# Kernel tuning notes

Measured on AMD Instinct MI355X. Metric: run time of the kernel, lower is better.

The kernel has to match this reference:

```python
import jax, jax.numpy as jnp
import numpy as np

BETA = 0.25

def setup_inputs() -> dict:
    key = jax.random.key(0)
    k1, k2 = jax.random.split(key)
    z = jax.random.normal(k1, (32, 64, 64, 64), dtype=jnp.float32)  # (B, D, H, W)
    # EmbeddingEMA init: uniform(-1/K, 1/K)
    K, D = 1024, 64
    weight = jax.random.uniform(k2, (K, D), dtype=jnp.float32, minval=-1.0 / K, maxval=1.0 / K)
    return {"z": z, "weight": weight}


def reference(z, weight):
    b, d, h, w = z.shape
    K = weight.shape[0]
    # permute (B,D,H,W) -> (B,H,W,D) and flatten to (N, D)
    z_flat = jnp.transpose(z, (0, 2, 3, 1)).reshape(-1, d)
    # squared euclidean distance: ||z||^2 + ||c||^2 - 2 z c^T  -> (N, K)
    distance = (
        jnp.sum(z_flat * z_flat, axis=1, keepdims=True)
        + jnp.sum(weight * weight, axis=1)
        - 2.0 * jnp.matmul(z_flat, weight.T)
    )
    vq_indices = jnp.argmin(distance, axis=1)  # (N,)
    z_quantized = weight[vq_indices]  # gather (N, D)
    # one-hot scatter stats (training-time EMA inputs)
    vq_current_count = jax.ops.segment_sum(
        jnp.ones((z_flat.shape[0],), dtype=z_flat.dtype), vq_indices, num_segments=K)
    vq_current_sum = jax.ops.segment_sum(z_flat, vq_indices, num_segments=K)  # (K, D)
    commitment_loss = jnp.mean((z_flat - jax.lax.stop_gradient(z_quantized)) ** 2)
    loss = BETA * commitment_loss
    # straight-through estimator
    q = z_flat + jax.lax.stop_gradient(z_quantized - z_flat)
    q = jnp.transpose(q.reshape(b, h, w, d), (0, 3, 1, 2))  # back to (B, D, H, W)
    return q, loss, commitment_loss, vq_current_count, vq_current_sum
```

## Files before the change

kernel.cpp:

```cpp
#include <hip/hip_runtime.h>


#define HWsz   4096
#define Dd     64
#define Kk     1024
#define NB     32
#define NTOT   131072
#define QSIZE  (NTOT * Dd)
#define BETA_C 0.25f

typedef float  f32x4  __attribute__((ext_vector_type(4)));
typedef short  bf16x8 __attribute__((ext_vector_type(8)));

__device__ __forceinline__ unsigned short f2bf(float f) {
    unsigned u = __float_as_uint(f);
    u += 0x7FFF + ((u >> 16) & 1);
    return (unsigned short)(u >> 16);
}
__device__ __forceinline__ float bf2f(unsigned short b) {
    return __uint_as_float(((unsigned)b) << 16);
}

__global__ __launch_bounds__(256) void vq_prep(const float* __restrict__ w,
                                               float* __restrict__ c2,
                                               unsigned short* __restrict__ whi,
                                               unsigned short* __restrict__ wlo) {
    int t = blockIdx.x * 256 + threadIdx.x;
    int k = t >> 6, d = t & 63;
    float v = w[t];
    unsigned short hb = f2bf(v);
    unsigned short lb = f2bf(v - bf2f(hb));
    int ctile = k >> 4, col = k & 15;
    int s = d >> 5, kg = (d >> 3) & 3, j = d & 7;
    int idx = (((ctile * 2 + s) * 64) + kg * 16 + col) * 8 + j;
    whi[idx] = hb; wlo[idx] = lb;

    if (t < Kk) {
        const float4* c4 = reinterpret_cast<const float4*>(w + t * Dd);
        float s0 = 0.f, s1 = 0.f, s2 = 0.f, s3 = 0.f;
#pragma unroll
        for (int q = 0; q < 16; ++q) {
            float4 cq = c4[q];
            s0 = fmaf(cq.x, cq.x, s0); s1 = fmaf(cq.y, cq.y, s1);
            s2 = fmaf(cq.z, cq.z, s2); s3 = fmaf(cq.w, cq.w, s3);
        }
        c2[t] = (s0 + s1) + (s2 + s3);
    }
}

__global__ __launch_bounds__(256) void vq_dist(const float* __restrict__ z,
                                               const float* __restrict__ w,
                                               const float* __restrict__ c2,
                                               const unsigned short* __restrict__ whi,
                                               const unsigned short* __restrict__ wlo,
                                               float* __restrict__ out,
                                               float* __restrict__ accum,
                                               int* __restrict__ idx_ws) {
    const int lane = threadIdx.x & 63;
    const int wid  = threadIdx.x >> 6;
    const int b    = blockIdx.x >> 4;
    const int t0   = (blockIdx.x & 15) * 16 + wid * 4;
    const int col  = lane & 15;
    const int kg   = lane >> 4;

    bf16x8 zhi[4][2], zlo[4][2];
#pragma unroll
    for (int m = 0; m < 4; ++m) {
        const int hw0 = (t0 + m) << 4;
        const float* zbase = z + (size_t)b * (Dd * HWsz) + hw0 + col;
#pragma unroll
        for (int s = 0; s < 2; ++s) {
            bf16x8 h, l;
#pragma unroll
            for (int j = 0; j < 8; ++j) {
                float zz = zbase[(size_t)(32 * s + kg * 8 + j) * HWsz];
                unsigned short hb = f2bf(zz);
                unsigned short lb = f2bf(zz - bf2f(hb));
                h[j] = (short)hb; l[j] = (short)lb;
            }
            zhi[m][s] = h; zlo[m][s] = l;
        }
    }

    float best[4][4];
    int   bk[4][4];
#pragma unroll
    for (int m = 0; m < 4; ++m)
#pragma unroll
        for (int r = 0; r < 4; ++r) { best[m][r] = 3.4e38f; bk[m][r] = 0; }

    const bf16x8* ph = reinterpret_cast<const bf16x8*>(whi);
    const bf16x8* pl = reinterpret_cast<const bf16x8*>(wlo);

    for (int ct = 0; ct < 64; ++ct) {
        bf16x8 wh0 = ph[(ct * 2 + 0) * 64 + lane];
        bf16x8 wh1 = ph[(ct * 2 + 1) * 64 + lane];
        bf16x8 wl0 = pl[(ct * 2 + 0) * 64 + lane];
        bf16x8 wl1 = pl[(ct * 2 + 1) * 64 + lane];

        float cv = c2[ct * 16 + col];
        int   kc = ct * 16 + col;

#pragma unroll
        for (int m = 0; m < 4; ++m) {
            f32x4 za = {0.f, 0.f, 0.f, 0.f};
            f32x4 zb = {0.f, 0.f, 0.f, 0.f};
            za = __builtin_amdgcn_mfma_f32_16x16x32_bf16(zhi[m][0], wh0, za, 0, 0, 0);
            za = __builtin_amdgcn_mfma_f32_16x16x32_bf16(zhi[m][1], wh1, za, 0, 0, 0);
            za = __builtin_amdgcn_mfma_f32_16x16x32_bf16(zhi[m][0], wl0, za, 0, 0, 0);
            za = __builtin_amdgcn_mfma_f32_16x16x32_bf16(zhi[m][1], wl1, za, 0, 0, 0);
            zb = __builtin_amdgcn_mfma_f32_16x16x32_bf16(zlo[m][0], wh0, zb, 0, 0, 0);
            zb = __builtin_amdgcn_mfma_f32_16x16x32_bf16(zlo[m][1], wh1, zb, 0, 0, 0);
#pragma unroll
            for (int r = 0; r < 4; ++r) {
                float s = fmaf(-2.f, za[r] + zb[r], cv);
                if (s < best[m][r]) { best[m][r] = s; bk[m][r] = kc; }
            }
        }
    }

#pragma unroll
    for (int off = 1; off < 16; off <<= 1) {
#pragma unroll
        for (int m = 0; m < 4; ++m)
#pragma unroll
            for (int r = 0; r < 4; ++r) {
                float ob = __shfl_xor(best[m][r], off, 64);
                int   ok = __shfl_xor(bk[m][r],   off, 64);
                if (ob < best[m][r] || (ob == best[m][r] && ok < bk[m][r])) {
                    best[m][r] = ob; bk[m][r] = ok;
                }
            }
    }

    float commit = 0.f;
    const int srcl = (col >> 2) << 4;
    const int rsel = col & 3;
#pragma unroll
    for (int m = 0; m < 4; ++m) {
        int c0 = __shfl(bk[m][0], srcl, 64);
        int c1 = __shfl(bk[m][1], srcl, 64);
        int c2r = __shfl(bk[m][2], srcl, 64);
        int c3 = __shfl(bk[m][3], srcl, 64);
        int mybk = (rsel == 0) ? c0 : (rsel == 1) ? c1 : (rsel == 2) ? c2r : c3;

        const int hw0 = (t0 + m) << 4;
        if (lane < 16) idx_ws[(size_t)b * HWsz + hw0 + col] = mybk;

        float* qbase = out + (size_t)b * (Dd * HWsz) + hw0 + col;
#pragma unroll
        for (int s = 0; s < 2; ++s) {
            const float4* cw = reinterpret_cast<const float4*>(w + mybk * Dd + 32 * s + kg * 8);
            float4 p0 = cw[0], p1 = cw[1];
            float cb[8] = {p0.x, p0.y, p0.z, p0.w, p1.x, p1.y, p1.z, p1.w};
#pragma unroll
            for (int j = 0; j < 8; ++j) {
                int   d  = 32 * s + kg * 8 + j;
                float zz = bf2f((unsigned short)zhi[m][s][j]) +
                           bf2f((unsigned short)zlo[m][s][j]);
                float cc = cb[j];
                qbase[(size_t)d * HWsz] = zz + (cc - zz);
                float dd = zz - cc;
                commit = fmaf(dd, dd, commit);
            }
        }
    }

#pragma unroll
    for (int off = 32; off > 0; off >>= 1) commit += __shfl_down(commit, off, 64);

    __shared__ float red[4];
    if (lane == 0) red[wid] = commit;
    __syncthreads();
    if (threadIdx.x == 0)
        atomicAdd(accum, (red[0] + red[1]) + (red[2] + red[3]));
}

__global__ __launch_bounds__(256) void vq_stats(const float* __restrict__ z,
                                                const int* __restrict__ idx_ws,
                                                float* __restrict__ psum,
                                                float* __restrict__ pcnt) {
    const int b     = blockIdx.x >> 3;
    const int chunk = blockIdx.x & 7;
    const int dbase = chunk * 8;
    const bool docnt = (chunk == 0);

    __shared__ float acc[8][Kk];
    __shared__ float cnt[Kk];
    for (int i = threadIdx.x; i < 8 * Kk; i += 256)
        acc[i >> 10][i & 1023] = 0.f;
    for (int i = threadIdx.x; i < Kk; i += 256) cnt[i] = 0.f;
    __syncthreads();

    const int4* ip = reinterpret_cast<const int4*>(idx_ws + (size_t)b * HWsz);
#pragma unroll
    for (int it = 0; it < 4; ++it) {
        int c4 = it * 256 + threadIdx.x;
        int4 k4 = ip[c4];
#pragma unroll
        for (int d8 = 0; d8 < 8; ++d8) {
            const float4 v4 = reinterpret_cast<const float4*>(
                z + ((size_t)b * Dd + dbase + d8) * HWsz)[c4];
            atomicAdd(&acc[d8][k4.x], v4.x);
            atomicAdd(&acc[d8][k4.y], v4.y);
            atomicAdd(&acc[d8][k4.z], v4.z);
            atomicAdd(&acc[d8][k4.w], v4.w);
        }
        if (docnt) {
            atomicAdd(&cnt[k4.x], 1.f);
            atomicAdd(&cnt[k4.y], 1.f);
            atomicAdd(&cnt[k4.z], 1.f);
            atomicAdd(&cnt[k4.w], 1.f);
        }
    }
    __syncthreads();

    float* po = psum + (size_t)b * (Dd * Kk) + (size_t)dbase * Kk;
    for (int i = threadIdx.x; i < 8 * Kk; i += 256)
        po[i] = acc[i >> 10][i & 1023];
    if (docnt) {
        float* pc = pcnt + (size_t)b * Kk;
        for (int i = threadIdx.x; i < Kk; i += 256) pc[i] = cnt[i];
    }
}

__global__ __launch_bounds__(256) void vq_reduce(const float* __restrict__ psum,
                                                 const float* __restrict__ pcnt,
                                                 const float* __restrict__ accum,
                                                 float* __restrict__ out) {
    int t = blockIdx.x * 256 + threadIdx.x;
    int k = t & 1023, d = t >> 10;
    float s = 0.f;
#pragma unroll
    for (int b = 0; b < NB; ++b)
        s += psum[(size_t)b * (Dd * Kk) + (size_t)d * Kk + k];
    out[QSIZE + 2 + Kk + (size_t)k * Dd + d] = s;
    if (t < Kk) {
        float c = 0.f;
#pragma unroll
        for (int b = 0; b < NB; ++b) c += pcnt[((size_t)b << 10) + t];
        out[QSIZE + 2 + t] = c;
    }
    if (t == 0) {
        float c = accum[0] / (float)QSIZE;
        out[QSIZE]     = BETA_C * c;
        out[QSIZE + 1] = c;
    }
}

extern "C" void kernel_launch(void* const* d_in, const int* in_sizes, int n_in,
                              void* d_out, int out_size, void* d_ws, size_t ws_size,
                              hipStream_t stream) {
    const float* z = (const float*)d_in[0];
    const float* w = (const float*)d_in[1];
    float* out = (float*)d_out;

    float* accum = (float*)d_ws;
    float* c2    = (float*)d_ws + 64;
    unsigned short* whi = (unsigned short*)((float*)d_ws + 64 + Kk);
    unsigned short* wlo = whi + (Kk * Dd);
    int*   idx_ws = (int*)(wlo + (Kk * Dd));
    float* psum   = (float*)(idx_ws + NTOT);
    float* pcnt   = psum + (size_t)NB * Dd * Kk;

    hipMemsetAsync(accum, 0, 64 * sizeof(float), stream);

    vq_prep<<<(Kk * Dd) / 256, 256, 0, stream>>>(w, c2, whi, wlo);
    vq_dist<<<NTOT / 256, 256, 0, stream>>>(z, w, c2, whi, wlo, out, accum, idx_ws);
    vq_stats<<<NB * 8, 256, 0, stream>>>(z, idx_ws, psum, pcnt);
    vq_reduce<<<(Kk * Dd) / 256, 256, 0, stream>>>(psum, pcnt, accum, out);
}
```

Baseline: 243.0 us.

## Stage codebook in LDS with double buffering and restructure dist/stats kernels

The distance kernel now runs 128-thread blocks that double-buffer the split-bf16 codebook chunks into LDS via global_load_lds. It interleaves MFMAs across four independent accumulators for more instruction-level parallelism and drops the separate zlo accumulator. The global atomic plus memset for the commitment loss is replaced by per-block partials reduced in the final kernel. The stats kernel is split finer, two D channels per block, giving more blocks and less LDS per block. This trades extra barriers and smaller blocks for less global-load latency on the codebook and better occupancy.

```diff
diff --git a/kernel.cpp b/kernel.cpp
--- a/kernel.cpp
+++ b/kernel.cpp
@@ -8,6 +8,8 @@
 #define NTOT   131072
 #define QSIZE  (NTOT * Dd)
 #define BETA_C 0.25f
+#define DIST_BLOCKS 1024
+#define NCHUNK 16
 
 typedef float  f32x4  __attribute__((ext_vector_type(4)));
 typedef short  bf16x8 __attribute__((ext_vector_type(8)));
@@ -19,6 +21,16 @@
 }
 __device__ __forceinline__ float bf2f(unsigned short b) {
     return __uint_as_float(((unsigned)b) << 16);
+}
+
+__device__ __forceinline__ void stage16(const void* g, void* lds, int lane) {
+#if __has_builtin(__builtin_amdgcn_global_load_lds)
+    __builtin_amdgcn_global_load_lds(
+        (const __attribute__((address_space(1))) unsigned int*)g,
+        (__attribute__((address_space(3))) unsigned int*)lds, 16, 0, 0);
+#else
+    *(bf16x8*)((unsigned short*)lds + lane * 8) = *(const bf16x8*)g;
+#endif
 }
 
 __global__ __launch_bounds__(256) void vq_prep(const float* __restrict__ w,
@@ -48,26 +60,27 @@
     }
 }
 
-__global__ __launch_bounds__(256) void vq_dist(const float* __restrict__ z,
-                                               const float* __restrict__ w,
-                                               const float* __restrict__ c2,
-                                               const unsigned short* __restrict__ whi,
-                                               const unsigned short* __restrict__ wlo,
-                                               float* __restrict__ out,
-                                               float* __restrict__ accum,
-                                               int* __restrict__ idx_ws) {
+__global__ __launch_bounds__(128, 3) void vq_dist(const float* __restrict__ z,
+                                                  const float* __restrict__ w,
+                                                  const float* __restrict__ c2,
+                                                  const unsigned short* __restrict__ whi,
+                                                  const unsigned short* __restrict__ wlo,
+                                                  float* __restrict__ out,
+                                                  float* __restrict__ commit_ws,
+                                                  int* __restrict__ idx_ws) {
     const int lane = threadIdx.x & 63;
     const int wid  = threadIdx.x >> 6;
-    const int b    = blockIdx.x >> 4;
-    const int t0   = (blockIdx.x & 15) * 16 + wid * 4;
+    const int b    = blockIdx.x >> 5;
+    const int hwb  = (blockIdx.x & 31) * 128 + wid * 64;
     const int col  = lane & 15;
     const int kg   = lane >> 4;
 
+    __shared__ unsigned short lbuf[2][8192];
+
     bf16x8 zhi[4][2], zlo[4][2];
 #pragma unroll
     for (int m = 0; m < 4; ++m) {
-        const int hw0 = (t0 + m) << 4;
-        const float* zbase = z + (size_t)b * (Dd * HWsz) + hw0 + col;
+        const float* zbase = z + (size_t)b * (Dd * HWsz) + (hwb + m * 16) + col;
 #pragma unroll
         for (int s = 0; s < 2; ++s) {
             bf16x8 h, l;
@@ -82,6 +95,19 @@
         }
     }
 
+    const char* ghi = (const char*)whi;
+    const char* glo = (const char*)wlo;
+#define STAGE(c, bufi)                                                          \
+    {                                                                           \
+        unsigned short* dst = lbuf[bufi];                                       \
+        _Pragma("unroll")                                                       \
+        for (int rd = 0; rd < 4; ++rd) {                                        \
+            int rec = ((c) * 8 + rd * 2 + wid) * 1024 + lane * 16;              \
+            stage16(ghi + rec, dst + rd * 2048 + wid * 512, lane);              \
+            stage16(glo + rec, dst + rd * 2048 + (2 + wid) * 512, lane);        \
+        }                                                                       \
+    }
+
     float best[4][4];
     int   bk[4][4];
 #pragma unroll
@@ -89,34 +115,53 @@
 #pragma unroll
         for (int r = 0; r < 4; ++r) { best[m][r] = 3.4e38f; bk[m][r] = 0; }
 
-    const bf16x8* ph = reinterpret_cast<const bf16x8*>(whi);
-    const bf16x8* pl = reinterpret_cast<const bf16x8*>(wlo);
-
-    for (int ct = 0; ct < 64; ++ct) {
-        bf16x8 wh0 = ph[(ct * 2 + 0) * 64 + lane];
-        bf16x8 wh1 = ph[(ct * 2 + 1) * 64 + lane];
-        bf16x8 wl0 = pl[(ct * 2 + 0) * 64 + lane];
-        bf16x8 wl1 = pl[(ct * 2 + 1) * 64 + lane];
-
-        float cv = c2[ct * 16 + col];
-        int   kc = ct * 16 + col;
-
-#pragma unroll
-        for (int m = 0; m < 4; ++m) {
-            f32x4 za = {0.f, 0.f, 0.f, 0.f};
-            f32x4 zb = {0.f, 0.f, 0.f, 0.f};
-            za = __builtin_amdgcn_mfma_f32_16x16x32_bf16(zhi[m][0], wh0, za, 0, 0, 0);
-            za = __builtin_amdgcn_mfma_f32_16x16x32_bf16(zhi[m][1], wh1, za, 0, 0, 0);
-            za = __builtin_amdgcn_mfma_f32_16x16x32_bf16(zhi[m][0], wl0, za, 0, 0, 0);
-            za = __builtin_amdgcn_mfma_f32_16x16x32_bf16(zhi[m][1], wl1, za, 0, 0, 0);
-            zb = __builtin_amdgcn_mfma_f32_16x16x32_bf16(zlo[m][0], wh0, zb, 0, 0, 0);
-            zb = __builtin_amdgcn_mfma_f32_16x16x32_bf16(zlo[m][1], wh1, zb, 0, 0, 0);
-#pragma unroll
-            for (int r = 0; r < 4; ++r) {
-                float s = fmaf(-2.f, za[r] + zb[r], cv);
-                if (s < best[m][r]) { best[m][r] = s; bk[m][r] = kc; }
-            }
-        }
+    STAGE(0, 0);
+    __syncthreads();
+
+    for (int c = 0; c < NCHUNK; ++c) {
+        const unsigned short* cb = lbuf[c & 1];
+        if (c + 1 < NCHUNK) STAGE(c + 1, (c + 1) & 1);
+#pragma unroll
+        for (int t = 0; t < 4; ++t) {
+            const int ct = c * 4 + t;
+            bf16x8 wh0 = *(const bf16x8*)(cb + t * 2048 + 0 * 512 + lane * 8);
+            bf16x8 wh1 = *(const bf16x8*)(cb + t * 2048 + 1 * 512 + lane * 8);
+            bf16x8 wl0 = *(const bf16x8*)(cb + t * 2048 + 2 * 512 + lane * 8);
+            bf16x8 wl1 = *(const bf16x8*)(cb + t * 2048 + 3 * 512 + lane * 8);
+            const float cv = c2[ct * 16 + col];
+            const int   kc = ct * 16 + col;
+
+            f32x4 za[4];
+#pragma unroll
+            for (int m = 0; m < 4; ++m) za[m] = (f32x4){0.f, 0.f, 0.f, 0.f};
+#pragma unroll
+            for (int m = 0; m < 4; ++m)
+                za[m] = __builtin_amdgcn_mfma_f32_16x16x32_bf16(zhi[m][0], wh0, za[m], 0, 0, 0);
+#pragma unroll
+            for (int m = 0; m < 4; ++m)
+                za[m] = __builtin_amdgcn_mfma_f32_16x16x32_bf16(zhi[m][1], wh1, za[m], 0, 0, 0);
+#pragma unroll
+            for (int m = 0; m < 4; ++m)
+                za[m] = __builtin_amdgcn_mfma_f32_16x16x32_bf16(zhi[m][0], wl0, za[m], 0, 0, 0);
+#pragma unroll
+            for (int m = 0; m < 4; ++m)
+                za[m] = __builtin_amdgcn_mfma_f32_16x16x32_bf16(zhi[m][1], wl1, za[m], 0, 0, 0);
+#pragma unroll
+            for (int m = 0; m < 4; ++m)
+                za[m] = __builtin_amdgcn_mfma_f32_16x16x32_bf16(zlo[m][0], wh0, za[m], 0, 0, 0);
+#pragma unroll
+            for (int m = 0; m < 4; ++m)
+                za[m] = __builtin_amdgcn_mfma_f32_16x16x32_bf16(zlo[m][1], wh1, za[m], 0, 0, 0);
+
+#pragma unroll
+            for (int m = 0; m < 4; ++m)
+#pragma unroll
+                for (int r = 0; r < 4; ++r) {
+                    float s = fmaf(-2.f, za[m][r], cv);
+                    if (s < best[m][r]) { best[m][r] = s; bk[m][r] = kc; }
+                }
+        }
+        __syncthreads();
     }
 
 #pragma unroll
@@ -144,7 +189,7 @@
         int c3 = __shfl(bk[m][3], srcl, 64);
         int mybk = (rsel == 0) ? c0 : (rsel == 1) ? c1 : (rsel == 2) ? c2r : c3;
 
-        const int hw0 = (t0 + m) << 4;
+        const int hw0 = hwb + m * 16;
         if (lane < 16) idx_ws[(size_t)b * HWsz + hw0 + col] = mybk;
 
         float* qbase = out + (size_t)b * (Dd * HWsz) + hw0 + col;
@@ -152,13 +197,13 @@
         for (int s = 0; s < 2; ++s) {
             const float4* cw = reinterpret_cast<const float4*>(w + mybk * Dd + 32 * s + kg * 8);
             float4 p0 = cw[0], p1 = cw[1];
-            float cb[8] = {p0.x, p0.y, p0.z, p0.w, p1.x, p1.y, p1.z, p1.w};
+            float cbv[8] = {p0.x, p0.y, p0.z, p0.w, p1.x, p1.y, p1.z, p1.w};
 #pragma unroll
             for (int j = 0; j < 8; ++j) {
                 int   d  = 32 * s + kg * 8 + j;
                 float zz = bf2f((unsigned short)zhi[m][s][j]) +
                            bf2f((unsigned short)zlo[m][s][j]);
-                float cc = cb[j];
+                float cc = cbv[j];
                 qbase[(size_t)d * HWsz] = zz + (cc - zz);
                 float dd = zz - cc;
                 commit = fmaf(dd, dd, commit);
@@ -169,55 +214,47 @@
 #pragma unroll
     for (int off = 32; off > 0; off >>= 1) commit += __shfl_down(commit, off, 64);
 
-    __shared__ float red[4];
+    __shared__ float red[2];
     if (lane == 0) red[wid] = commit;
     __syncthreads();
-    if (threadIdx.x == 0)
-        atomicAdd(accum, (red[0] + red[1]) + (red[2] + red[3]));
+    if (threadIdx.x == 0) commit_ws[blockIdx.x] = red[0] + red[1];
 }
 
 __global__ __launch_bounds__(256) void vq_stats(const float* __restrict__ z,
                                                 const int* __restrict__ idx_ws,
                                                 float* __restrict__ psum,
                                                 float* __restrict__ pcnt) {
-    const int b     = blockIdx.x >> 3;
-    const int chunk = blockIdx.x & 7;
-    const int dbase = chunk * 8;
-    const bool docnt = (chunk == 0);
-
-    __shared__ float acc[8][Kk];
-    __shared__ float cnt[Kk];
-    for (int i = threadIdx.x; i < 8 * Kk; i += 256)
-        acc[i >> 10][i & 1023] = 0.f;
-    for (int i = threadIdx.x; i < Kk; i += 256) cnt[i] = 0.f;
+    const int b  = blockIdx.x >> 5;
+    const int dp = blockIdx.x & 31;
+    const int d0 = dp * 2;
+    const bool docnt = (dp == 0);
+
+    __shared__ float acc0[Kk], acc1[Kk], cnt[Kk];
+    for (int i = threadIdx.x; i < Kk; i += 256) { acc0[i] = 0.f; acc1[i] = 0.f; cnt[i] = 0.f; }
     __syncthreads();
 
-    const int4* ip = reinterpret_cast<const int4*>(idx_ws + (size_t)b * HWsz);
+    const int4*   ip  = reinterpret_cast<const int4*>(idx_ws + (size_t)b * HWsz);
+    const float4* zp0 = reinterpret_cast<const float4*>(z + ((size_t)b * Dd + d0) * HWsz);
+    const float4* zp1 = reinterpret_cast<const float4*>(z + ((size_t)b * Dd + d0 + 1) * HWsz);
 #pragma unroll
     for (int it = 0; it < 4; ++it) {
         int c4 = it * 256 + threadIdx.x;
-        int4 k4 = ip[c4];
-#pragma unroll
-        for (int d8 = 0; d8 < 8; ++d8) {
-            const float4 v4 = reinterpret_cast<const float4*>(
-                z + ((size_t)b * Dd + dbase + d8) * HWsz)[c4];
-            atomicAdd(&acc[d8][k4.x], v4.x);
-            atomicAdd(&acc[d8][k4.y], v4.y);
-            atomicAdd(&acc[d8][k4.z], v4.z);
-            atomicAdd(&acc[d8][k4.w], v4.w);
-        }
+        int4   k4 = ip[c4];
+        float4 v0 = zp0[c4];
+        float4 v1 = zp1[c4];
+        atomicAdd(&acc0[k4.x], v0.x); atomicAdd(&acc0[k4.y], v0.y);
+        atomicAdd(&acc0[k4.z], v0.z); atomicAdd(&acc0[k4.w], v0.w);
+        atomicAdd(&acc1[k4.x], v1.x); atomicAdd(&acc1[k4.y], v1.y);
+        atomicAdd(&acc1[k4.z], v1.z); atomicAdd(&acc1[k4.w], v1.w);
         if (docnt) {
-            atomicAdd(&cnt[k4.x], 1.f);
-            atomicAdd(&cnt[k4.y], 1.f);
-            atomicAdd(&cnt[k4.z], 1.f);
-            atomicAdd(&cnt[k4.w], 1.f);
+            atomicAdd(&cnt[k4.x], 1.f); atomicAdd(&cnt[k4.y], 1.f);
+            atomicAdd(&cnt[k4.z], 1.f); atomicAdd(&cnt[k4.w], 1.f);
         }
     }
     __syncthreads();
 
-    float* po = psum + (size_t)b * (Dd * Kk) + (size_t)dbase * Kk;
-    for (int i = threadIdx.x; i < 8 * Kk; i += 256)
-        po[i] = acc[i >> 10][i & 1023];
+    float* po = psum + ((size_t)b * Dd + d0) * Kk;
+    for (int i = threadIdx.x; i < Kk; i += 256) { po[i] = acc0[i]; po[Kk + i] = acc1[i]; }
     if (docnt) {
         float* pc = pcnt + (size_t)b * Kk;
         for (int i = threadIdx.x; i < Kk; i += 256) pc[i] = cnt[i];
@@ -226,14 +263,14 @@
 
 __global__ __launch_bounds__(256) void vq_reduce(const float* __restrict__ psum,
                                                  const float* __restrict__ pcnt,
-                                                 const float* __restrict__ accum,
+                                                 const float* __restrict__ commit_ws,
                                                  float* __restrict__ out) {
     int t = blockIdx.x * 256 + threadIdx.x;
     int k = t & 1023, d = t >> 10;
     float s = 0.f;
 #pragma unroll
     for (int b = 0; b < NB; ++b)
-        s += psum[(size_t)b * (Dd * Kk) + (size_t)d * Kk + k];
+        s += psum[((size_t)b * Dd + d) * Kk + k];
     out[QSIZE + 2 + Kk + (size_t)k * Dd + d] = s;
     if (t < Kk) {
         float c = 0.f;
@@ -241,10 +278,21 @@
         for (int b = 0; b < NB; ++b) c += pcnt[((size_t)b << 10) + t];
         out[QSIZE + 2 + t] = c;
     }
-    if (t == 0) {
-        float c = accum[0] / (float)QSIZE;
-        out[QSIZE]     = BETA_C * c;
-        out[QSIZE + 1] = c;
+
+    if (blockIdx.x == 0) {
+        float cs = 0.f;
+        for (int i = threadIdx.x; i < DIST_BLOCKS; i += 256) cs += commit_ws[i];
+#pragma unroll
+        for (int off = 32; off > 0; off >>= 1) cs += __shfl_down(cs, off, 64);
+        __shared__ float r2[4];
+        const int lane = threadIdx.x & 63, wid = threadIdx.x >> 6;
+        if (lane == 0) r2[wid] = cs;
+        __syncthreads();
+        if (threadIdx.x == 0) {
+            float c = ((r2[0] + r2[1]) + (r2[2] + r2[3])) / (float)QSIZE;
+            out[QSIZE]     = BETA_C * c;
+            out[QSIZE + 1] = c;
+        }
     }
 }
 
@@ -255,18 +303,16 @@
     const float* w = (const float*)d_in[1];
     float* out = (float*)d_out;
 
-    float* accum = (float*)d_ws;
-    float* c2    = (float*)d_ws + 64;
-    unsigned short* whi = (unsigned short*)((float*)d_ws + 64 + Kk);
+    float* commit_ws = (float*)d_ws;
+    float* c2        = (float*)d_ws + 1024;
+    unsigned short* whi = (unsigned short*)((float*)d_ws + 2048);
     unsigned short* wlo = whi + (Kk * Dd);
     int*   idx_ws = (int*)(wlo + (Kk * Dd));
-    float* psum   = (float*)(idx_ws + NTOT);
-    float* pcnt   = psum + (size_t)NB * Dd * Kk;
-
-    hipMemsetAsync(accum, 0, 64 * sizeof(float), stream);
+    float* pcnt   = (float*)(idx_ws + NTOT);
+    float* psum   = pcnt + (size_t)NB * Kk;
 
     vq_prep<<<(Kk * Dd) / 256, 256, 0, stream>>>(w, c2, whi, wlo);
-    vq_dist<<<NTOT / 256, 256, 0, stream>>>(z, w, c2, whi, wlo, out, accum, idx_ws);
-    vq_stats<<<NB * 8, 256, 0, stream>>>(z, idx_ws, psum, pcnt);
-    vq_reduce<<<(Kk * Dd) / 256, 256, 0, stream>>>(psum, pcnt, accum, out);
-}
+    vq_dist<<<DIST_BLOCKS, 128, 0, stream>>>(z, w, c2, whi, wlo, out, commit_ws, idx_ws);
+    vq_stats<<<NB * 32, 256, 0, stream>>>(z, idx_ws, psum, pcnt);
+    vq_reduce<<<(Kk * Dd) / 256, 256, 0, stream>>>(psum, pcnt, commit_ws, out);
+}
```

Measured after the change: 236.1 us. 1.03x faster.
